# Optimization experiments

Hardware: AMD Instinct MI355X
Metric: run time of the kernel (lower is better)

The kernel has to match this reference:

```python
import jax, jax.numpy as jnp
import numpy as np

N = 50000   # n_nodes
E = 800000  # n_edges
R = 8       # n_relations
D = 64      # in_feats
H = 2       # num_heads
K = 32      # attention_feats
NEG_SLOPE = 0.2


def setup_inputs() -> dict:
    key = jax.random.key(0)
    ks = jax.random.split(key, 11)
    feat = jax.random.normal(ks[0], (N, D), jnp.float32)
    W_src = jax.random.normal(ks[1], (R, D, H * K), jnp.float32) * 0.05
    b_src = jax.random.normal(ks[2], (R, H * K), jnp.float32) * 0.05
    qual_table = jax.random.normal(ks[3], (N, D), jnp.float32)  # node_quality embedding
    W_qual = jax.random.normal(ks[4], (R, D, H * K), jnp.float32) * 0.05
    b_qual = jax.random.normal(ks[5], (R, H * K), jnp.float32) * 0.05
    attn = jax.random.normal(ks[6], (R, H, K), jnp.float32) * 0.05
    src = jax.random.randint(ks[7], (E,), 0, N)
    dst = jax.random.randint(ks[8], (E,), 0, N)
    r_type = jax.random.randint(ks[9], (E,), 0, R)
    nid = jax.random.randint(ks[10], (E,), 0, N)
    return dict(feat=feat, W_src=W_src, b_src=b_src, qual_table=qual_table,
                W_qual=W_qual, b_qual=b_qual, attn=attn,
                src=src, dst=dst, r_type=r_type, nid=nid)


def reference(feat, W_src, b_src, qual_table, W_qual, b_qual, attn, src, dst, r_type, nid):
    # Relation-specific projection. Mathematically identical to per-edge
    # gather_mm(h[idx], W, idx_b=r_type): precompute all (node, relation)
    # projections (N*R*H*K is small) then gather per edge.
    proj_src = jnp.einsum('nd,rdk->nrk', feat, W_src)          # (N, R, H*K)
    el = (proj_src[src, r_type] + b_src[r_type]).reshape(E, H, K)
    proj_q = jnp.einsum('nd,rdk->nrk', qual_table, W_qual)     # (N, R, H*K)
    qual = (proj_q[nid, r_type] + b_qual[r_type]).reshape(E, H, K)

    e = jax.nn.leaky_relu(el + qual, negative_slope=NEG_SLOPE)  # (E, H, K)
    scores = jnp.sum(e * attn[r_type], axis=-1)                 # (E, H)

    # edge_softmax over incoming edges of each destination node
    smax = jax.ops.segment_max(scores, dst, num_segments=N)     # (N, H)
    z = jnp.exp(scores - smax[dst])
    denom = jax.ops.segment_sum(z, dst, num_segments=N)         # (N, H)
    a = z / denom[dst]                                          # (E, H)

    # narre: messages use the raw source features h_src, broadcast over heads
    m = feat[src][:, None, :] * a[:, :, None]                   # (E, H, D)
    rst = jax.ops.segment_sum(m, dst, num_segments=N)           # (N, H, D)
    return rst
```

## Files before the change

kernel.cpp:

```cpp
#include <hip/hip_runtime.h>
#include <hip/hip_bf16.h>
#include <cstdint>


__device__ __forceinline__ int rfl(int v) { return __builtin_amdgcn_readfirstlane(v); }

typedef __attribute__((ext_vector_type(8))) short bf16x8;
typedef __attribute__((ext_vector_type(4))) float f32x4;

#define CTR_STRIDE 16
#define RCAP 131072
#define BCAP 4864

__device__ __forceinline__ uint32_t pk2(float a, float b) {
  uint32_t ua = __float_as_uint(a) + 0x8000u;
  uint32_t ub = __float_as_uint(b) + 0x8000u;
  return __builtin_amdgcn_perm(ub, ua, 0x07060302u);
}

__device__ __forceinline__ float dpp_add16(float x) {
  float s = x;
  int t;
  t = __builtin_amdgcn_update_dpp(0, __float_as_int(s), 0x128, 0xF, 0xF, true);
  s += __int_as_float(t);
  t = __builtin_amdgcn_update_dpp(0, __float_as_int(s), 0x124, 0xF, 0xF, true);
  s += __int_as_float(t);
  t = __builtin_amdgcn_update_dpp(0, __float_as_int(s), 0x122, 0xF, 0xF, true);
  s += __int_as_float(t);
  t = __builtin_amdgcn_update_dpp(0, __float_as_int(s), 0x121, 0xF, 0xF, true);
  s += __int_as_float(t);
  return s;
}

__device__ __forceinline__ void rel_mask_rank(bool valid, int r, int lane,
                                              uint64_t& m, int& rank) {
  const uint64_t b0 = __ballot(valid && (r & 1));
  const uint64_t b1 = __ballot(valid && (r & 2));
  const uint64_t b2 = __ballot(valid && (r & 4));
  const uint64_t vv = __ballot(valid);
  m = vv;
  m &= (r & 1) ? b0 : ~b0;
  m &= (r & 2) ? b1 : ~b1;
  m &= (r & 4) ? b2 : ~b2;
  rank = (int)__popcll(m & (((uint64_t)1 << lane) - 1));
}

__global__ void prep_k(const float* __restrict__ Wsrc, const float* __restrict__ Wqual,
                       ushort* __restrict__ Wt,
                       const float* __restrict__ feat, const float* __restrict__ qual,
                       ushort* __restrict__ feat_bf, ushort* __restrict__ qual_bf,
                       long tabElems, int convB,
                       int* __restrict__ cursor_r, int* __restrict__ bkt_cur, int nbkt) {
  const int bx = blockIdx.x;
  if (bx < convB) {
    const long gt = (long)bx * 1024 + threadIdx.x;
    const long be = gt * 8;
    if (be < 2 * tabElems) {
      const int m = be >= tabElems;
      const long off = be - (m ? tabElems : 0);
      const float* s = (m ? qual : feat) + off;
      uint32_t o[4];
#pragma unroll
      for (int i = 0; i < 4; ++i) o[i] = pk2(s[2 * i], s[2 * i + 1]);
      *(uint4*)((m ? qual_bf : feat_bf) + off) = make_uint4(o[0], o[1], o[2], o[3]);
    }
    return;
  }
  if (bx < convB + 4) {
    const int gt = (bx - convB) * 1024 + threadIdx.x;
    const int m = gt >> 11;
    const int r = (gt >> 8) & 7;
    const int col = (gt >> 2) & 63;
    const int k0 = (gt & 3) * 16;
    const float* W = (m ? Wqual : Wsrc) + (size_t)r * 4096;
    uint32_t o[8];
#pragma unroll
    for (int i = 0; i < 8; ++i) {
      float a = W[(k0 + 2 * i) * 64 + col];
      float b = W[(k0 + 2 * i + 1) * 64 + col];
      o[i] = pk2(a, b);
    }
    ushort* d = Wt + ((((size_t)m * 8 + r) * 64 + col) * 64 + k0);
    *(uint4*)d = make_uint4(o[0], o[1], o[2], o[3]);
    *(uint4*)(d + 8) = make_uint4(o[4], o[5], o[6], o[7]);
    return;
  }
  const int t = threadIdx.x;
  if (t < 8) cursor_r[t * CTR_STRIDE] = t * RCAP;
  if (t >= 8 && t < 8 + nbkt) bkt_cur[(t - 8) * CTR_STRIDE] = (t - 8) * BCAP;
}

__global__ __launch_bounds__(1024) void pass1_k(
    const int* __restrict__ src, const int* __restrict__ dst,
    const int* __restrict__ rt, const int* __restrict__ nid,
    int* __restrict__ cursor_r, int* __restrict__ bkt_cur,
    int* __restrict__ src_r, int* __restrict__ nid_r,
    uint2* __restrict__ recs, int E) {
  __shared__ int wcnt[16][8];
  __shared__ int wbase[16][8];
  __shared__ int lhist[256];
  __shared__ int gbase[256];
  const int tid = threadIdx.x;
  const int wid = tid >> 6;
  const int lane = tid & 63;
  if (lane < 8) wcnt[wid][lane] = 0;
  if (tid < 256) lhist[tid] = 0;
  __syncthreads();
  const int e = blockIdx.x * 1024 + tid;
  const bool valid = e < E;
  int r = 0, d = 0, b = 0, lpos = 0;
  if (valid) {
    r = rt[e];
    d = dst[e];
    b = d >> 8;
    lpos = atomicAdd(&lhist[b], 1);
  }
  uint64_t m;
  int rank;
  rel_mask_rank(valid, r, lane, m, rank);
  if (valid && rank == 0) wcnt[wid][r] = (int)__popcll(m);
  __syncthreads();
  if (tid < 8) {
    int tot = 0;
#pragma unroll
    for (int w = 0; w < 16; ++w) tot += wcnt[w][tid];
    int run = tot ? atomicAdd(&cursor_r[tid * CTR_STRIDE], tot) : 0;
#pragma unroll
    for (int w = 0; w < 16; ++w) { wbase[w][tid] = run; run += wcnt[w][tid]; }
  }
  if (tid < 256) {
    const int c = lhist[tid];
    gbase[tid] = c ? atomicAdd(&bkt_cur[tid * CTR_STRIDE], c) : 0;
  }
  __syncthreads();
  if (valid) {
    const int p_r = wbase[wid][r] + rank;
    src_r[p_r] = src[e];
    nid_r[p_r] = nid[e];
    recs[gbase[b] + lpos] = make_uint2((uint32_t)d, (uint32_t)p_r);
  }
}

__global__ __launch_bounds__(1024) void pass2_k(const uint2* __restrict__ recs,
                                                const int* __restrict__ bkt_cur,
                                                int2* __restrict__ bc_d,
                                                int* __restrict__ perm_p, int N) {
  __shared__ int lcnt[256];
  __shared__ int soffs[256];
  __shared__ int wsum[4];
  __shared__ int wbase[4];
  const int b = blockIdx.x;
  const int dlo = b << 8;
  const int tid = threadIdx.x;
  const int lane = tid & 63;
  const int bstart = b * BCAP;
  const int bend = bkt_cur[b * CTR_STRIDE];
  if (tid < 256) lcnt[tid] = 0;
  __syncthreads();
  for (int i = bstart + tid; i < bend; i += 1024)
    atomicAdd(&lcnt[recs[i].x & 255u], 1);
  __syncthreads();
  int x = 0, v = 0;
  if (tid < 256) {
    v = lcnt[tid];
    x = v;
#pragma unroll
    for (int off = 1; off < 64; off <<= 1) {
      int y = __shfl_up(x, off);
      if (lane >= off) x += y;
    }
    if (lane == 63) wsum[tid >> 6] = x;
  }
  __syncthreads();
  if (tid == 0) {
    int run = 0;
#pragma unroll
    for (int w = 0; w < 4; ++w) { wbase[w] = run; run += wsum[w]; }
  }
  __syncthreads();
  if (tid < 256) {
    const int st = bstart + x - v + wbase[tid >> 6];
    soffs[tid] = st;
    const int d = dlo + tid;
    if (d < N) bc_d[d] = make_int2(st, v);
    lcnt[tid] = 0;
  }
  __syncthreads();
  for (int i = bstart + tid; i < bend; i += 1024) {
    const uint2 rec = recs[i];
    const int ld = (int)(rec.x & 255u);
    const int rank = atomicAdd(&lcnt[ld], 1);
    perm_p[soffs[ld] + rank] = (int)rec.y;
  }
}

__global__ __launch_bounds__(256, 8) void score_k(
    const ushort* __restrict__ feat_bf, const ushort* __restrict__ qual_bf,
    const ushort* __restrict__ Wt,
    const float* __restrict__ bsrc, const float* __restrict__ bqual,
    const float* __restrict__ attn,
    const int* __restrict__ src_r, const int* __restrict__ nid_r,
    uint4* __restrict__ rec_sa) {
  __shared__ __align__(16) ushort lT[2][64 * 64];
  __shared__ float comb[4][128];

  const int tid = threadIdx.x;
  const int lane = tid & 63;
  const int wid = tid >> 6;
  const int base = blockIdx.x * 128;
  const int r = blockIdx.x >> 10;
  if (rfl(src_r[base]) < 0) return;

  const int col = wid * 16 + (lane & 15);
  const int kb = (lane >> 4) * 8;
  const ushort* WtS = Wt + ((size_t)r * 64 + col) * 64;
  const ushort* WtQ = Wt + (((size_t)8 + r) * 64 + col) * 64;
  const bf16x8 wS0 = *(const bf16x8*)(WtS + kb);
  const bf16x8 wS1 = *(const bf16x8*)(WtS + 32 + kb);
  const bf16x8 wQ0 = *(const bf16x8*)(WtQ + kb);
  const bf16x8 wQ1 = *(const bf16x8*)(WtQ + 32 + kb);
  const float bias_l = bsrc[r * 64 + col] + bqual[r * 64 + col];
  const float attn_l = attn[r * 64 + col];

  for (int sb = 0; sb < 2; ++sb) {
    {
      const int m = tid >> 7;
      const int es = (tid >> 1) & 63;
      const int hf = tid & 1;
      const int gs = base + sb * 64 + es;
      const int sv = src_r[gs];
      char* dp = (char*)(lT[m] + es * 64);
      const int swz = (es & 7) << 4;
      if (sv >= 0) {
        const int node = m ? nid_r[gs] : sv;
        const char* gp = (const char*)(m ? qual_bf : feat_bf) + (size_t)node * 128 + hf * 64;
#pragma unroll
        for (int c = 0; c < 4; ++c)
          *(uint4*)(dp + ((hf * 64 + c * 16) ^ swz)) = *(const uint4*)(gp + c * 16);
      } else {
        uint4 z = make_uint4(0, 0, 0, 0);
#pragma unroll
        for (int c = 0; c < 4; ++c) *(uint4*)(dp + ((hf * 64 + c * 16) ^ swz)) = z;
      }
    }
    __syncthreads();

#pragma unroll
    for (int et = 0; et < 4; ++et) {
      const int row = et * 16 + (lane & 15);
      const int rb = row * 128;
      const int swz = (row & 7) << 4;
      const int k0 = (lane >> 4) * 16;
      bf16x8 aS0 = *(const bf16x8*)((const char*)lT[0] + rb + (k0 ^ swz));
      bf16x8 aS1 = *(const bf16x8*)((const char*)lT[0] + rb + ((k0 + 64) ^ swz));
      bf16x8 aQ0 = *(const bf16x8*)((const char*)lT[1] + rb + (k0 ^ swz));
      bf16x8 aQ1 = *(const bf16x8*)((const char*)lT[1] + rb + ((k0 + 64) ^ swz));
      f32x4 acc = {0.f, 0.f, 0.f, 0.f};
      acc = __builtin_amdgcn_mfma_f32_16x16x32_bf16(aS0, wS0, acc, 0, 0, 0);
      acc = __builtin_amdgcn_mfma_f32_16x16x32_bf16(aS1, wS1, acc, 0, 0, 0);
      acc = __builtin_amdgcn_mfma_f32_16x16x32_bf16(aQ0, wQ0, acc, 0, 0, 0);
      acc = __builtin_amdgcn_mfma_f32_16x16x32_bf16(aQ1, wQ1, acc, 0, 0, 0);

      float p0, p1, p2, p3;
#pragma unroll
      for (int j = 0; j < 4; ++j) {
        float v = acc[j] + bias_l;
        v = v > 0.f ? v : 0.2f * v;
        float s = dpp_add16(v * attn_l);
        if (j == 0) p0 = s; else if (j == 1) p1 = s; else if (j == 2) p2 = s; else p3 = s;
      }
      const int sub = lane & 15;
      if (sub < 4) {
        float v = sub == 0 ? p0 : sub == 1 ? p1 : sub == 2 ? p2 : p3;
        comb[wid][sb * 64 + et * 16 + (lane >> 4) * 4 + sub] = v;
      }
    }
    __syncthreads();
  }

  if (tid < 128) {
    const int gs = base + tid;
    rec_sa[gs] = make_uint4(__float_as_uint(comb[0][tid] + comb[1][tid]),
                            __float_as_uint(comb[2][tid] + comb[3][tid]),
                            (uint32_t)src_r[gs], 0u);
  }
}

__global__ __launch_bounds__(256) void agg_k(
    const ushort* __restrict__ feat_bf, const uint4* __restrict__ rec_sa,
    const int* __restrict__ perm_p, const int2* __restrict__ bc_d,
    float* __restrict__ out, int N, int nquads) {
  const int lane = threadIdx.x & 63;
  const int wid = threadIdx.x >> 6;
  const int g = lane >> 4;
  const int gl = lane & 15;
  const int gbase = g << 4;

  for (int q = blockIdx.x * 4 + wid; q < nquads; q += 2048 * 4) {
    const int n = q * 4 + g;
    if (n >= N) continue;
    const int2 bc = bc_d[n];
    const int beg = bc.x;
    const int cnt = bc.y;
    float A0[4] = {0.f, 0.f, 0.f, 0.f};
    float A1[4] = {0.f, 0.f, 0.f, 0.f};
    float d0 = 0.f, d1 = 0.f;

    if (cnt > 0 && cnt <= 32) {
      const bool v0 = gl < cnt;
      const bool v1 = gl + 16 < cnt;
      float sx0 = -3.4e38f, sy0 = -3.4e38f, sx1 = -3.4e38f, sy1 = -3.4e38f;
      int sl0 = 0, sl1 = 0;
      if (v0) {
        const uint4 rec = rec_sa[perm_p[beg + gl]];
        sx0 = __uint_as_float(rec.x); sy0 = __uint_as_float(rec.y); sl0 = (int)rec.z;
      }
      if (v1) {
        const uint4 rec = rec_sa[perm_p[beg + 16 + gl]];
        sx1 = __uint_as_float(rec.x); sy1 = __uint_as_float(rec.y); sl1 = (int)rec.z;
      }
      float m0 = fmaxf(sx0, sx1), m1 = fmaxf(sy0, sy1);
#pragma unroll
      for (int off = 8; off; off >>= 1) {
        m0 = fmaxf(m0, __shfl_xor(m0, off));
        m1 = fmaxf(m1, __shfl_xor(m1, off));
      }
      const float z0a = v0 ? __expf(sx0 - m0) : 0.f;
      const float z1a = v0 ? __expf(sy0 - m1) : 0.f;
      const float z0b = v1 ? __expf(sx1 - m0) : 0.f;
      const float z1b = v1 ? __expf(sy1 - m1) : 0.f;
      d0 = z0a + z0b;
      d1 = z1a + z1b;
#pragma unroll 4
      for (int k = 0; k < cnt; ++k) {
        const int srcl = gbase + (k & 15);
        const int hi = k >> 4;
        const int ss = __shfl(hi ? sl1 : sl0, srcl);
        const float w0 = __shfl(hi ? z0b : z0a, srcl);
        const float w1 = __shfl(hi ? z1b : z1a, srcl);
        const uint2 fv = *(const uint2*)(feat_bf + (size_t)ss * 64 + (gl << 2));
        const float f0 = __uint_as_float(fv.x << 16);
        const float f1 = __uint_as_float(fv.x & 0xffff0000u);
        const float f2 = __uint_as_float(fv.y << 16);
        const float f3 = __uint_as_float(fv.y & 0xffff0000u);
        A0[0] = fmaf(f0, w0, A0[0]); A0[1] = fmaf(f1, w0, A0[1]);
        A0[2] = fmaf(f2, w0, A0[2]); A0[3] = fmaf(f3, w0, A0[3]);
        A1[0] = fmaf(f0, w1, A1[0]); A1[1] = fmaf(f1, w1, A1[1]);
        A1[2] = fmaf(f2, w1, A1[2]); A1[3] = fmaf(f3, w1, A1[3]);
      }
    } else if (cnt > 32) {
      float m0 = -3.4e38f, m1 = -3.4e38f;
      for (int i = gl; i < cnt; i += 16) {
        const uint4 rec = rec_sa[perm_p[beg + i]];
        m0 = fmaxf(m0, __uint_as_float(rec.x));
        m1 = fmaxf(m1, __uint_as_float(rec.y));
      }
#pragma unroll
      for (int off = 8; off; off >>= 1) {
        m0 = fmaxf(m0, __shfl_xor(m0, off));
        m1 = fmaxf(m1, __shfl_xor(m1, off));
      }
      for (int c0 = 0; c0 < cnt; c0 += 16) {
        const int i = c0 + gl;
        const bool val = i < cnt;
        int sl = 0;
        float z0 = 0.f, z1 = 0.f;
        if (val) {
          const uint4 rec = rec_sa[perm_p[beg + i]];
          z0 = __expf(__uint_as_float(rec.x) - m0);
          z1 = __expf(__uint_as_float(rec.y) - m1);
          sl = (int)rec.z;
        }
        d0 += z0;
        d1 += z1;
        const int kmax = min(16, cnt - c0);
#pragma unroll 4
        for (int k = 0; k < kmax; ++k) {
          const int srcl = gbase + k;
          const int ss = __shfl(sl, srcl);
          const float w0 = __shfl(z0, srcl);
          const float w1 = __shfl(z1, srcl);
          const uint2 fv = *(const uint2*)(feat_bf + (size_t)ss * 64 + (gl << 2));
          const float f0 = __uint_as_float(fv.x << 16);
          const float f1 = __uint_as_float(fv.x & 0xffff0000u);
          const float f2 = __uint_as_float(fv.y << 16);
          const float f3 = __uint_as_float(fv.y & 0xffff0000u);
          A0[0] = fmaf(f0, w0, A0[0]); A0[1] = fmaf(f1, w0, A0[1]);
          A0[2] = fmaf(f2, w0, A0[2]); A0[3] = fmaf(f3, w0, A0[3]);
          A1[0] = fmaf(f0, w1, A1[0]); A1[1] = fmaf(f1, w1, A1[1]);
          A1[2] = fmaf(f2, w1, A1[2]); A1[3] = fmaf(f3, w1, A1[3]);
        }
      }
    }
#pragma unroll
    for (int off = 8; off; off >>= 1) {
      d0 += __shfl_xor(d0, off);
      d1 += __shfl_xor(d1, off);
    }
    const float r0 = (cnt > 0) ? 1.f / d0 : 0.f;
    const float r1 = (cnt > 0) ? 1.f / d1 : 0.f;
    float4 s0 = make_float4(A0[0] * r0, A0[1] * r0, A0[2] * r0, A0[3] * r0);
    float4 s1 = make_float4(A1[0] * r1, A1[1] * r1, A1[2] * r1, A1[3] * r1);
    *(float4*)(out + (size_t)n * 128 + (gl << 2)) = s0;
    *(float4*)(out + (size_t)n * 128 + 64 + (gl << 2)) = s1;
  }
}

extern "C" void kernel_launch(void* const* d_in, const int* in_sizes, int n_in,
                              void* d_out, int out_size, void* d_ws, size_t ws_size,
                              hipStream_t stream) {
  const float* feat  = (const float*)d_in[0];
  const float* Wsrc  = (const float*)d_in[1];
  const float* bsrc  = (const float*)d_in[2];
  const float* qual  = (const float*)d_in[3];
  const float* Wqual = (const float*)d_in[4];
  const float* bqual = (const float*)d_in[5];
  const float* attn  = (const float*)d_in[6];
  const int* src = (const int*)d_in[7];
  const int* dst = (const int*)d_in[8];
  const int* rt  = (const int*)d_in[9];
  const int* nid = (const int*)d_in[10];
  float* out = (float*)d_out;

  const int N = in_sizes[0] / 64;
  const int E = in_sizes[7];
  const long tabElems = (long)N * 64;
  const int NBKT = (N + 255) / 256;
  const size_t RSLOTS = (size_t)8 * RCAP;

  char* p = (char*)d_ws;
  int* cursor_r = (int*)p;      p += 8 * CTR_STRIDE * 4;
  int* bkt_cur = (int*)p;       p += (size_t)NBKT * CTR_STRIDE * 4;
  int2* bc_d = (int2*)p;        p += (size_t)N * 8;
  int* src_r = (int*)p;         p += RSLOTS * 4;
  int* nid_r = (int*)p;         p += RSLOTS * 4;
  uint2* recs = (uint2*)p;      p += (size_t)NBKT * BCAP * 8;
  int* perm_p = (int*)p;        p += (size_t)NBKT * BCAP * 4;
  ushort* Wt = (ushort*)p;      p += 2 * 8 * 64 * 64 * 2;
  ushort* feat_bf = (ushort*)p; p += (size_t)tabElems * 2;
  ushort* qual_bf = (ushort*)p; p += (size_t)tabElems * 2;
  uint4* rec_sa = (uint4*)p;    p += RSLOTS * 16;
  if ((size_t)(p - (char*)d_ws) > ws_size) return;

  hipMemsetAsync(src_r, 0xFF, RSLOTS * 4, stream);

  const int convB = (int)((2 * tabElems / 8 + 1023) / 1024);
  prep_k<<<convB + 5, 1024, 0, stream>>>(Wsrc, Wqual, Wt, feat, qual, feat_bf, qual_bf,
                                         tabElems, convB, cursor_r, bkt_cur, NBKT);
  pass1_k<<<(E + 1023) / 1024, 1024, 0, stream>>>(src, dst, rt, nid, cursor_r, bkt_cur,
                                                  src_r, nid_r, recs, E);
  pass2_k<<<NBKT, 1024, 0, stream>>>(recs, bkt_cur, bc_d, perm_p, N);
  score_k<<<(int)(RSLOTS / 128), 256, 0, stream>>>(feat_bf, qual_bf, Wt, bsrc, bqual, attn,
                                                   src_r, nid_r, rec_sa);
  const int nquads = (N + 3) / 4;
  const int aggB = min(2048, (nquads + 3) / 4);
  agg_k<<<aggB, 256, 0, stream>>>(feat_bf, rec_sa, perm_p, bc_d, out, N, nquads);
}
```

Measured before the change: 135.2 us.

## Merge preprocessing kernels into two launches with counters zeroed by memset

The bf16 conversion and weight transpose blocks now run in the same launch as the pass1 edge binning. The per-destination bucket sort (pass2) shares a launch with the relation-sorted scoring kernel, running as extra 256-thread blocks. Counters are now zero-initialised by a memset and offsets are computed relative to the bucket or relation base. The aim is to cut launch count and let independent work overlap. In exchange, pass2 blocks use fewer threads per bucket and run alongside the scoring blocks.

```diff
diff --git a/kernel.cpp b/kernel.cpp
--- a/kernel.cpp
+++ b/kernel.cpp
@@ -45,15 +45,39 @@
   rank = (int)__popcll(m & (((uint64_t)1 << lane) - 1));
 }
 
-__global__ void prep_k(const float* __restrict__ Wsrc, const float* __restrict__ Wqual,
-                       ushort* __restrict__ Wt,
-                       const float* __restrict__ feat, const float* __restrict__ qual,
-                       ushort* __restrict__ feat_bf, ushort* __restrict__ qual_bf,
-                       long tabElems, int convB,
-                       int* __restrict__ cursor_r, int* __restrict__ bkt_cur, int nbkt) {
+__global__ __launch_bounds__(1024) void fused1_k(
+    const int* __restrict__ src, const int* __restrict__ dst,
+    const int* __restrict__ rt, const int* __restrict__ nid,
+    int* __restrict__ cursor_r, int* __restrict__ bkt_cur,
+    int* __restrict__ src_r, int* __restrict__ nid_r,
+    uint2* __restrict__ recs, int E, int p1B,
+    const float* __restrict__ Wsrc, const float* __restrict__ Wqual,
+    ushort* __restrict__ Wt,
+    const float* __restrict__ feat, const float* __restrict__ qual,
+    ushort* __restrict__ feat_bf, ushort* __restrict__ qual_bf,
+    long tabElems, int convB) {
   const int bx = blockIdx.x;
-  if (bx < convB) {
-    const long gt = (long)bx * 1024 + threadIdx.x;
+  if (bx >= p1B + convB) {
+    const int gt = (bx - p1B - convB) * 1024 + threadIdx.x;
+    const int m = gt >> 11;
+    const int r = (gt >> 8) & 7;
+    const int col = (gt >> 2) & 63;
+    const int k0 = (gt & 3) * 16;
+    const float* W = (m ? Wqual : Wsrc) + (size_t)r * 4096;
+    uint32_t o[8];
+#pragma unroll
+    for (int i = 0; i < 8; ++i) {
+      float a = W[(k0 + 2 * i) * 64 + col];
+      float b = W[(k0 + 2 * i + 1) * 64 + col];
+      o[i] = pk2(a, b);
+    }
+    ushort* d = Wt + ((((size_t)m * 8 + r) * 64 + col) * 64 + k0);
+    *(uint4*)d = make_uint4(o[0], o[1], o[2], o[3]);
+    *(uint4*)(d + 8) = make_uint4(o[4], o[5], o[6], o[7]);
+    return;
+  }
+  if (bx >= p1B) {
+    const long gt = (long)(bx - p1B) * 1024 + threadIdx.x;
     const long be = gt * 8;
     if (be < 2 * tabElems) {
       const int m = be >= tabElems;
@@ -66,36 +90,6 @@
     }
     return;
   }
-  if (bx < convB + 4) {
-    const int gt = (bx - convB) * 1024 + threadIdx.x;
-    const int m = gt >> 11;
-    const int r = (gt >> 8) & 7;
-    const int col = (gt >> 2) & 63;
-    const int k0 = (gt & 3) * 16;
-    const float* W = (m ? Wqual : Wsrc) + (size_t)r * 4096;
-    uint32_t o[8];
-#pragma unroll
-    for (int i = 0; i < 8; ++i) {
-      float a = W[(k0 + 2 * i) * 64 + col];
-      float b = W[(k0 + 2 * i + 1) * 64 + col];
-      o[i] = pk2(a, b);
-    }
-    ushort* d = Wt + ((((size_t)m * 8 + r) * 64 + col) * 64 + k0);
-    *(uint4*)d = make_uint4(o[0], o[1], o[2], o[3]);
-    *(uint4*)(d + 8) = make_uint4(o[4], o[5], o[6], o[7]);
-    return;
-  }
-  const int t = threadIdx.x;
-  if (t < 8) cursor_r[t * CTR_STRIDE] = t * RCAP;
-  if (t >= 8 && t < 8 + nbkt) bkt_cur[(t - 8) * CTR_STRIDE] = (t - 8) * BCAP;
-}
-
-__global__ __launch_bounds__(1024) void pass1_k(
-    const int* __restrict__ src, const int* __restrict__ dst,
-    const int* __restrict__ rt, const int* __restrict__ nid,
-    int* __restrict__ cursor_r, int* __restrict__ bkt_cur,
-    int* __restrict__ src_r, int* __restrict__ nid_r,
-    uint2* __restrict__ recs, int E) {
   __shared__ int wcnt[16][8];
   __shared__ int wbase[16][8];
   __shared__ int lhist[256];
@@ -106,7 +100,7 @@
   if (lane < 8) wcnt[wid][lane] = 0;
   if (tid < 256) lhist[tid] = 0;
   __syncthreads();
-  const int e = blockIdx.x * 1024 + tid;
+  const int e = bx * 1024 + tid;
   const bool valid = e < E;
   int r = 0, d = 0, b = 0, lpos = 0;
   if (valid) {
@@ -134,77 +128,75 @@
   }
   __syncthreads();
   if (valid) {
-    const int p_r = wbase[wid][r] + rank;
+    const int p_r = r * RCAP + wbase[wid][r] + rank;
     src_r[p_r] = src[e];
     nid_r[p_r] = nid[e];
-    recs[gbase[b] + lpos] = make_uint2((uint32_t)d, (uint32_t)p_r);
-  }
-}
-
-__global__ __launch_bounds__(1024) void pass2_k(const uint2* __restrict__ recs,
-                                                const int* __restrict__ bkt_cur,
-                                                int2* __restrict__ bc_d,
-                                                int* __restrict__ perm_p, int N) {
-  __shared__ int lcnt[256];
-  __shared__ int soffs[256];
-  __shared__ int wsum[4];
-  __shared__ int wbase[4];
-  const int b = blockIdx.x;
-  const int dlo = b << 8;
-  const int tid = threadIdx.x;
-  const int lane = tid & 63;
-  const int bstart = b * BCAP;
-  const int bend = bkt_cur[b * CTR_STRIDE];
-  if (tid < 256) lcnt[tid] = 0;
-  __syncthreads();
-  for (int i = bstart + tid; i < bend; i += 1024)
-    atomicAdd(&lcnt[recs[i].x & 255u], 1);
-  __syncthreads();
-  int x = 0, v = 0;
-  if (tid < 256) {
-    v = lcnt[tid];
-    x = v;
-#pragma unroll
-    for (int off = 1; off < 64; off <<= 1) {
-      int y = __shfl_up(x, off);
-      if (lane >= off) x += y;
-    }
-    if (lane == 63) wsum[tid >> 6] = x;
-  }
-  __syncthreads();
-  if (tid == 0) {
-    int run = 0;
-#pragma unroll
-    for (int w = 0; w < 4; ++w) { wbase[w] = run; run += wsum[w]; }
-  }
-  __syncthreads();
-  if (tid < 256) {
-    const int st = bstart + x - v + wbase[tid >> 6];
-    soffs[tid] = st;
-    const int d = dlo + tid;
-    if (d < N) bc_d[d] = make_int2(st, v);
-    lcnt[tid] = 0;
-  }
-  __syncthreads();
-  for (int i = bstart + tid; i < bend; i += 1024) {
-    const uint2 rec = recs[i];
-    const int ld = (int)(rec.x & 255u);
-    const int rank = atomicAdd(&lcnt[ld], 1);
-    perm_p[soffs[ld] + rank] = (int)rec.y;
-  }
-}
-
-__global__ __launch_bounds__(256, 8) void score_k(
+    recs[(size_t)b * BCAP + gbase[b] + lpos] = make_uint2((uint32_t)d, (uint32_t)p_r);
+  }
+}
+
+__global__ __launch_bounds__(256, 8) void fused2_k(
     const ushort* __restrict__ feat_bf, const ushort* __restrict__ qual_bf,
     const ushort* __restrict__ Wt,
     const float* __restrict__ bsrc, const float* __restrict__ bqual,
     const float* __restrict__ attn,
     const int* __restrict__ src_r, const int* __restrict__ nid_r,
-    uint4* __restrict__ rec_sa) {
-  __shared__ __align__(16) ushort lT[2][64 * 64];
-  __shared__ float comb[4][128];
-
+    uint4* __restrict__ rec_sa, int scoreB,
+    const uint2* __restrict__ recs, const int* __restrict__ bkt_cur,
+    int2* __restrict__ bc_d, int* __restrict__ perm_p, int N) {
+  __shared__ __align__(16) char smem[18432];
   const int tid = threadIdx.x;
+
+  if ((int)blockIdx.x >= scoreB) {
+    int* lcnt = (int*)smem;
+    int* soffs = (int*)(smem + 1024);
+    int* wsum = (int*)(smem + 2048);
+    int* wb2 = (int*)(smem + 2064);
+    const int b = blockIdx.x - scoreB;
+    const int dlo = b << 8;
+    const int lane = tid & 63;
+    const int bstart = b * BCAP;
+    const int bend = bstart + bkt_cur[b * CTR_STRIDE];
+    lcnt[tid] = 0;
+    __syncthreads();
+    for (int i = bstart + tid; i < bend; i += 256)
+      atomicAdd(&lcnt[recs[i].x & 255u], 1);
+    __syncthreads();
+    int v = lcnt[tid];
+    int x = v;
+#pragma unroll
+    for (int off = 1; off < 64; off <<= 1) {
+      int y = __shfl_up(x, off);
+      if (lane >= off) x += y;
+    }
+    if (lane == 63) wsum[tid >> 6] = x;
+    __syncthreads();
+    if (tid == 0) {
+      int run = 0;
+#pragma unroll
+      for (int w = 0; w < 4; ++w) { wb2[w] = run; run += wsum[w]; }
+    }
+    __syncthreads();
+    {
+      const int st = bstart + x - v + wb2[tid >> 6];
+      soffs[tid] = st;
+      const int d = dlo + tid;
+      if (d < N) bc_d[d] = make_int2(st, v);
+      lcnt[tid] = 0;
+    }
+    __syncthreads();
+    for (int i = bstart + tid; i < bend; i += 256) {
+      const uint2 rec = recs[i];
+      const int ld = (int)(rec.x & 255u);
+      const int rank = atomicAdd(&lcnt[ld], 1);
+      perm_p[soffs[ld] + rank] = (int)rec.y;
+    }
+    return;
+  }
+
+  ushort* lT0 = (ushort*)smem;
+  ushort* lT1 = (ushort*)(smem + 8192);
+  float* comb = (float*)(smem + 16384);
   const int lane = tid & 63;
   const int wid = tid >> 6;
   const int base = blockIdx.x * 128;
@@ -229,7 +221,7 @@
       const int hf = tid & 1;
       const int gs = base + sb * 64 + es;
       const int sv = src_r[gs];
-      char* dp = (char*)(lT[m] + es * 64);
+      char* dp = (char*)((m ? lT1 : lT0) + es * 64);
       const int swz = (es & 7) << 4;
       if (sv >= 0) {
         const int node = m ? nid_r[gs] : sv;
@@ -251,10 +243,10 @@
       const int rb = row * 128;
       const int swz = (row & 7) << 4;
       const int k0 = (lane >> 4) * 16;
-      bf16x8 aS0 = *(const bf16x8*)((const char*)lT[0] + rb + (k0 ^ swz));
-      bf16x8 aS1 = *(const bf16x8*)((const char*)lT[0] + rb + ((k0 + 64) ^ swz));
-      bf16x8 aQ0 = *(const bf16x8*)((const char*)lT[1] + rb + (k0 ^ swz));
-      bf16x8 aQ1 = *(const bf16x8*)((const char*)lT[1] + rb + ((k0 + 64) ^ swz));
+      bf16x8 aS0 = *(const bf16x8*)((const char*)lT0 + rb + (k0 ^ swz));
+      bf16x8 aS1 = *(const bf16x8*)((const char*)lT0 + rb + ((k0 + 64) ^ swz));
+      bf16x8 aQ0 = *(const bf16x8*)((const char*)lT1 + rb + (k0 ^ swz));
+      bf16x8 aQ1 = *(const bf16x8*)((const char*)lT1 + rb + ((k0 + 64) ^ swz));
       f32x4 acc = {0.f, 0.f, 0.f, 0.f};
       acc = __builtin_amdgcn_mfma_f32_16x16x32_bf16(aS0, wS0, acc, 0, 0, 0);
       acc = __builtin_amdgcn_mfma_f32_16x16x32_bf16(aS1, wS1, acc, 0, 0, 0);
@@ -272,7 +264,7 @@
       const int sub = lane & 15;
       if (sub < 4) {
         float v = sub == 0 ? p0 : sub == 1 ? p1 : sub == 2 ? p2 : p3;
-        comb[wid][sb * 64 + et * 16 + (lane >> 4) * 4 + sub] = v;
+        comb[wid * 128 + sb * 64 + et * 16 + (lane >> 4) * 4 + sub] = v;
       }
     }
     __syncthreads();
@@ -280,8 +272,8 @@
 
   if (tid < 128) {
     const int gs = base + tid;
-    rec_sa[gs] = make_uint4(__float_as_uint(comb[0][tid] + comb[1][tid]),
-                            __float_as_uint(comb[2][tid] + comb[3][tid]),
+    rec_sa[gs] = make_uint4(__float_as_uint(comb[0 * 128 + tid] + comb[1 * 128 + tid]),
+                            __float_as_uint(comb[2 * 128 + tid] + comb[3 * 128 + tid]),
                             (uint32_t)src_r[gs], 0u);
   }
 }
@@ -442,16 +434,20 @@
   uint4* rec_sa = (uint4*)p;    p += RSLOTS * 16;
   if ((size_t)(p - (char*)d_ws) > ws_size) return;
 
+  hipMemsetAsync(cursor_r, 0, (size_t)(8 + NBKT) * CTR_STRIDE * 4, stream);
   hipMemsetAsync(src_r, 0xFF, RSLOTS * 4, stream);
 
+  const int p1B = (E + 1023) / 1024;
   const int convB = (int)((2 * tabElems / 8 + 1023) / 1024);
-  prep_k<<<convB + 5, 1024, 0, stream>>>(Wsrc, Wqual, Wt, feat, qual, feat_bf, qual_bf,
-                                         tabElems, convB, cursor_r, bkt_cur, NBKT);
-  pass1_k<<<(E + 1023) / 1024, 1024, 0, stream>>>(src, dst, rt, nid, cursor_r, bkt_cur,
-                                                  src_r, nid_r, recs, E);
-  pass2_k<<<NBKT, 1024, 0, stream>>>(recs, bkt_cur, bc_d, perm_p, N);
-  score_k<<<(int)(RSLOTS / 128), 256, 0, stream>>>(feat_bf, qual_bf, Wt, bsrc, bqual, attn,
-                                                   src_r, nid_r, rec_sa);
+  fused1_k<<<p1B + convB + 4, 1024, 0, stream>>>(src, dst, rt, nid, cursor_r, bkt_cur,
+                                                 src_r, nid_r, recs, E, p1B,
+                                                 Wsrc, Wqual, Wt,
+                                                 feat, qual, feat_bf, qual_bf,
+                                                 tabElems, convB);
+  const int scoreB = (int)(RSLOTS / 128);
+  fused2_k<<<scoreB + NBKT, 256, 0, stream>>>(feat_bf, qual_bf, Wt, bsrc, bqual, attn,
+                                              src_r, nid_r, rec_sa, scoreB,
+                                              recs, bkt_cur, bc_d, perm_p, N);
   const int nquads = (N + 3) / 4;
   const int aggB = min(2048, (nquads + 3) / 4);
   agg_k<<<aggB, 256, 0, stream>>>(feat_bf, rec_sa, perm_p, bc_d, out, N, nquads);
```

Result: faster. 132.1 us (-2.2%).
